# Optimization experiments

Measured on AMD Instinct MI355X. Metric: run time of the kernel, lower is better.

## Reference

```python
import jax, jax.numpy as jnp
import numpy as np

C_IN = 256
C_OUT = 256


def setup_inputs() -> dict:
    key = jax.random.key(0)
    k1, k2, k3, k4, k5 = jax.random.split(key, 5)
    B, C, H, W = 4, C_IN, 64, 64
    x = jax.random.normal(k1, (B, C, H, W), dtype=jnp.float32)
    y = jax.random.normal(k2, (B, C, H, W), dtype=jnp.float32)
    s = 1.0 / np.sqrt(C_IN)  # kaiming-ish init scale for 1x1 conv
    wq = jax.random.normal(k3, (C_OUT, C_IN), dtype=jnp.float32) * s
    wk = jax.random.normal(k4, (C_OUT, C_IN), dtype=jnp.float32) * s
    wv = jax.random.normal(k5, (C_OUT, C_IN), dtype=jnp.float32) * s
    gamma = jnp.ones((1,), dtype=jnp.float32) * 0.1
    return {"x": x, "y": y, "wq": wq, "wk": wk, "wv": wv, "gamma": gamma}


def reference(x, y, wq, wk, wv, gamma):
    B, C, H, W = x.shape
    N = H * W
    xf = x.reshape(B, C, N)  # [B, C, N]
    yf = y.reshape(B, C, N)
    q = jnp.einsum('oc,bcn->bno', wq, xf)   # [B, N, Co]
    k = jnp.einsum('oc,bcn->bon', wk, yf)   # [B, Co, N]
    v = jnp.einsum('oc,bcn->bon', wv, yf)   # [B, Co, N]
    energy = jnp.einsum('bio,boj->bij', q, k)          # [B, N, N]
    attention = jax.nn.softmax(energy, axis=-1)
    out = jnp.einsum('bcj,bij->bci', v, attention)     # [B, Co, N]
    out = out.reshape(B, -1, H, W)
    return gamma[0] * out + x
```

## Files before the change

kernel.cpp:

```cpp
#include <hip/hip_runtime.h>
#include <hip/hip_bf16.h>
#include <stdint.h>

#define C_DIM 256
#define N_DIM 4096
#define B_DIM 4

typedef __attribute__((ext_vector_type(8))) short s16x8;
typedef __attribute__((ext_vector_type(4))) short s16x4;
typedef __attribute__((ext_vector_type(4))) float f32x4;
typedef __attribute__((ext_vector_type(16))) float f32x16;
typedef __attribute__((ext_vector_type(4))) int i32x4;

static __device__ __forceinline__ short f2bs(float f) {
    __bf16 h = (__bf16)f;
    return __builtin_bit_cast(short, h);
}
static __device__ __forceinline__ float bs2f(short s) {
    unsigned int u = ((unsigned int)(unsigned short)s) << 16;
    return __builtin_bit_cast(float, u);
}
static __device__ __forceinline__ unsigned cvtpk(float lo, float hi) {
    unsigned r;
    asm("v_cvt_pk_bf16_f32 %0, %1, %2" : "=v"(r) : "v"(lo), "v"(hi));
    return r;
}
static __device__ __forceinline__ void plswap(unsigned &a, unsigned &b) {
    asm("v_permlane32_swap_b32 %0, %1" : "+v"(a), "+v"(b));
}

__global__ __launch_bounds__(256)
void prep_kernel(const float* __restrict__ x, const float* __restrict__ y,
                 const float* __restrict__ wq, const float* __restrict__ wk,
                 const float* __restrict__ wv,
                 short* __restrict__ xT, short* __restrict__ yT,
                 short* __restrict__ wb)
{
    int bid = blockIdx.x;
    int t = threadIdx.x;
    if (bid < 2048) {
        const float* src = (bid < 1024) ? x : y;
        short* dst = (bid < 1024) ? xT : yT;
        int id = bid & 1023;
        int ct = id & 3;
        int nt = (id >> 2) & 63;
        int b  = id >> 8;
        int n0 = nt * 64, c0 = ct * 64;
        __shared__ short T[64][66];
        int l = t & 63;
        int wv_ = t >> 6;
        #pragma unroll
        for (int p = 0; p < 16; ++p) {
            int c = wv_ + p * 4;
            float v = src[((size_t)(b * C_DIM + c0 + c)) * N_DIM + n0 + l];
            T[l][c] = f2bs(v);
        }
        __syncthreads();
        #pragma unroll
        for (int p = 0; p < 16; ++p) {
            int n = wv_ + p * 4;
            dst[((size_t)(b * N_DIM + n0 + n)) * C_DIM + c0 + l] = T[n][l];
        }
    } else {
        int id = bid - 2048;
        const float* w = (id < 32) ? wq : (id < 64) ? wk : wv;
        short* dst = wb + (size_t)(id / 32) * (C_DIM * C_DIM);
        int off = (id & 31) * 2048 + t * 8;
        f32x4 a  = *(const f32x4*)(w + off);
        f32x4 b4 = *(const f32x4*)(w + off + 4);
        s16x8 r;
        r[0]=f2bs(a[0]);  r[1]=f2bs(a[1]);  r[2]=f2bs(a[2]);  r[3]=f2bs(a[3]);
        r[4]=f2bs(b4[0]); r[5]=f2bs(b4[1]); r[6]=f2bs(b4[2]); r[7]=f2bs(b4[3]);
        *(s16x8*)(dst + off) = r;
    }
}

__global__ __launch_bounds__(256)
void proj_kernel(const short* __restrict__ xT, const short* __restrict__ yT,
                 const short* __restrict__ wb,
                 short* __restrict__ Qb, short* __restrict__ Kb,
                 short* __restrict__ Vb)
{
    int bid = blockIdx.x;
    int ot = bid & 3;
    int nt = (bid >> 2) & 63;
    int bp = bid >> 8;
    int b = bp / 3, p = bp % 3;
    int n0 = nt * 64, o0 = ot * 64;
    const short* src = (p == 0) ? xT : yT;
    const short* w = wb + (size_t)p * C_DIM * C_DIM;

    __shared__ __align__(16) short Xs[64][264];
    __shared__ __align__(16) short Ws[64][264];

    int t = threadIdx.x;
    const short* srcb = src + (size_t)(b * N_DIM + n0) * C_DIM;
    const short* wsrc = w + (size_t)o0 * C_DIM;
    #pragma unroll
    for (int pas = 0; pas < 8; ++pas) {
        int slot = pas * 256 + t;
        int row = slot >> 5, ck = slot & 31;
        *(s16x8*)&Xs[row][ck * 8] = *(const s16x8*)&srcb[(size_t)row * C_DIM + ck * 8];
        *(s16x8*)&Ws[row][ck * 8] = *(const s16x8*)&wsrc[(size_t)row * C_DIM + ck * 8];
    }
    __syncthreads();

    int lane = t & 63;
    int wid = t >> 6;
    int m = lane & 15, q = lane >> 4;
    f32x4 acc[4] = {};

    if (p < 2) {
        #pragma unroll
        for (int kk = 0; kk < 8; ++kk) {
            s16x8 af = *(const s16x8*)&Xs[wid * 16 + m][kk * 32 + q * 8];
            #pragma unroll
            for (int ob = 0; ob < 4; ++ob) {
                s16x8 bf = *(const s16x8*)&Ws[ob * 16 + m][kk * 32 + q * 8];
                acc[ob] = __builtin_amdgcn_mfma_f32_16x16x32_bf16(af, bf, acc[ob], 0, 0, 0);
            }
        }
        float sc = (p == 0) ? 1.4426950408889634f : 1.0f;
        short* dst = ((p == 0) ? Qb : Kb) + (size_t)b * N_DIM * C_DIM;
        #pragma unroll
        for (int ob = 0; ob < 4; ++ob)
            #pragma unroll
            for (int r = 0; r < 4; ++r) {
                int n = n0 + wid * 16 + q * 4 + r;
                int o = o0 + ob * 16 + m;
                dst[(size_t)n * C_DIM + o] = f2bs(acc[ob][r] * sc);
            }
    } else {
        #pragma unroll
        for (int kk = 0; kk < 8; ++kk) {
            s16x8 af = *(const s16x8*)&Ws[wid * 16 + m][kk * 32 + q * 8];
            #pragma unroll
            for (int nb = 0; nb < 4; ++nb) {
                s16x8 bf = *(const s16x8*)&Xs[nb * 16 + m][kk * 32 + q * 8];
                acc[nb] = __builtin_amdgcn_mfma_f32_16x16x32_bf16(af, bf, acc[nb], 0, 0, 0);
            }
        }
        short* dst = Vb + (size_t)b * C_DIM * N_DIM;
        #pragma unroll
        for (int nb = 0; nb < 4; ++nb)
            #pragma unroll
            for (int r = 0; r < 4; ++r) {
                int o = o0 + wid * 16 + q * 4 + r;
                int n = n0 + nb * 16 + m;
                dst[(size_t)o * N_DIM + n] = f2bs(acc[nb][r]);
            }
    }
}

__global__ __launch_bounds__(256, 2)
void attn_kernel(const short* __restrict__ Qb, const short* __restrict__ Kb,
                 const short* __restrict__ Vb,
                 short* __restrict__ Op01, short* __restrict__ Op23,
                 float* __restrict__ ms)
{
    int bid0 = blockIdx.x;
    int swz = (bid0 & 7) * 64 + (bid0 >> 3);
    int b  = swz >> 7;
    int ks = (swz >> 5) & 3;
    int qt = swz & 31;
    int i0 = qt * 128;

    int t = threadIdx.x;
    int wv = t >> 6;
    int lane = t & 63;
    int il = lane & 31, hi = lane >> 5;
    int q0 = i0 + wv * 32;

    __shared__ __align__(16) short Ksh[32][264];
    __shared__ __align__(16) short Vsh[256][40];

    const short* Qp = Qb + (size_t)b * N_DIM * C_DIM;
    const short* Kp = Kb + (size_t)b * N_DIM * C_DIM + (size_t)(ks * 1024) * C_DIM;
    const short* Vp = Vb + (size_t)b * C_DIM * N_DIM + ks * 1024;

    s16x8 qf[16];
    {
        const short* qrow = Qp + (size_t)(q0 + il) * C_DIM + hi * 8;
        #pragma unroll
        for (int kk = 0; kk < 16; ++kk)
            qf[kk] = *(const s16x8*)&qrow[kk * 16];
    }

    int krb = t >> 5, kck = t & 31;
    int vrb = t >> 2, vck = t & 3;

    {
        s16x8 kr[4], vr[4];
        #pragma unroll
        for (int p = 0; p < 4; ++p)
            kr[p] = *(const s16x8*)&Kp[(size_t)(p * 8 + krb) * C_DIM + kck * 8];
        #pragma unroll
        for (int p = 0; p < 4; ++p)
            vr[p] = *(const s16x8*)&Vp[(size_t)(p * 64 + vrb) * N_DIM + vck * 8];
        #pragma unroll
        for (int p = 0; p < 4; ++p) *(s16x8*)&Ksh[p * 8 + krb][kck * 8] = kr[p];
        #pragma unroll
        for (int p = 0; p < 4; ++p) *(s16x8*)&Vsh[p * 64 + vrb][vck * 8] = vr[p];
    }
    __syncthreads();

    f32x16 acc[8] = {};
    float srun = 0.f;

    for (int jt = 0; jt < 32; ++jt) {
        bool pfch = (jt < 31);

        f32x16 sv0 = {}, sv1 = {};
        __builtin_amdgcn_s_setprio(1);
        #pragma unroll
        for (int kk = 0; kk < 8; ++kk) {
            s16x8 a0 = *(const s16x8*)&Ksh[il][kk * 16 + hi * 8];
            sv0 = __builtin_amdgcn_mfma_f32_32x32x16_bf16(a0, qf[kk], sv0, 0, 0, 0);
            s16x8 a1 = *(const s16x8*)&Ksh[il][(kk + 8) * 16 + hi * 8];
            sv1 = __builtin_amdgcn_mfma_f32_32x32x16_bf16(a1, qf[kk + 8], sv1, 0, 0, 0);
        }
        __builtin_amdgcn_s_setprio(0);

        s16x8 kr[4];
        if (pfch) {
            const short* kg = Kp + (size_t)((jt + 1) * 32) * C_DIM;
            #pragma unroll
            for (int p = 0; p < 4; ++p)
                kr[p] = *(const s16x8*)&kg[(size_t)(p * 8 + krb) * C_DIM + kck * 8];
        }

        #pragma unroll
        for (int r = 0; r < 16; ++r) {
            float pe = exp2f((sv0[r] + sv1[r]) - 64.f);
            sv0[r] = pe;
            srun += pe;
        }

        unsigned d0[4], d1[4];
        #pragma unroll
        for (int rq = 0; rq < 4; ++rq) {
            d0[rq] = cvtpk(sv0[4 * rq + 0], sv0[4 * rq + 1]);
            d1[rq] = cvtpk(sv0[4 * rq + 2], sv0[4 * rq + 3]);
        }
        unsigned w0a = d0[0], w2a = d0[1]; plswap(w0a, w2a);
        unsigned w1a = d1[0], w3a = d1[1]; plswap(w1a, w3a);
        unsigned w0b = d0[2], w2b = d0[3]; plswap(w0b, w2b);
        unsigned w1b = d1[2], w3b = d1[3]; plswap(w1b, w3b);
        i32x4 pi0 = { (int)w0a, (int)w1a, (int)w2a, (int)w3a };
        i32x4 pi1 = { (int)w0b, (int)w1b, (int)w2b, (int)w3b };
        s16x8 pf0 = __builtin_bit_cast(s16x8, pi0);
        s16x8 pf1 = __builtin_bit_cast(s16x8, pi1);

        s16x8 vr[4];
        if (pfch) {
            const short* vg = Vp + (jt + 1) * 32;
            #pragma unroll
            for (int p = 0; p < 4; ++p)
                vr[p] = *(const s16x8*)&vg[(size_t)(p * 64 + vrb) * N_DIM + vck * 8];
        }

        __builtin_amdgcn_s_setprio(1);
        #pragma unroll
        for (int cs = 0; cs < 8; ++cs) {
            s16x8 va = *(const s16x8*)&Vsh[cs * 32 + il][hi * 8];
            acc[cs] = __builtin_amdgcn_mfma_f32_32x32x16_bf16(va, pf0, acc[cs], 0, 0, 0);
            s16x8 vb = *(const s16x8*)&Vsh[cs * 32 + il][16 + hi * 8];
            acc[cs] = __builtin_amdgcn_mfma_f32_32x32x16_bf16(vb, pf1, acc[cs], 0, 0, 0);
        }
        __builtin_amdgcn_s_setprio(0);

        __syncthreads();
        if (pfch) {
            #pragma unroll
            for (int p = 0; p < 4; ++p) *(s16x8*)&Ksh[p * 8 + krb][kck * 8] = kr[p];
            #pragma unroll
            for (int p = 0; p < 4; ++p) *(s16x8*)&Vsh[p * 64 + vrb][vck * 8] = vr[p];
        }
        __syncthreads();
    }

    srun += __shfl_xor(srun, 32, 64);
    int i = q0 + il;
    const size_t HSZ = (size_t)B_DIM * C_DIM * N_DIM;
    if (ks < 2) {
        short* o = Op01 + (size_t)ks * HSZ + (size_t)(b * C_DIM) * N_DIM + i;
        #pragma unroll
        for (int cs = 0; cs < 8; ++cs)
            #pragma unroll
            for (int r = 0; r < 16; ++r) {
                int c = cs * 32 + (r & 3) + 8 * (r >> 2) + 4 * hi;
                o[(size_t)c * N_DIM] = f2bs(acc[cs][r]);
            }
    } else {
        short* o = Op23 + ((size_t)(b * C_DIM) * N_DIM + i) * 2 + (ks - 2);
        #pragma unroll
        for (int cs = 0; cs < 8; ++cs)
            #pragma unroll
            for (int r = 0; r < 16; ++r) {
                int c = cs * 32 + (r & 3) + 8 * (r >> 2) + 4 * hi;
                o[(size_t)c * N_DIM * 2] = f2bs(acc[cs][r]);
            }
    }
    if (hi == 0) {
        float* msp = ms + (size_t)(ks * B_DIM + b) * N_DIM;
        msp[i] = srun;
    }
}

__global__ __launch_bounds__(256)
void merge_kernel(const short* __restrict__ Op01, const short* Op23,
                  const float* __restrict__ ms, const float* __restrict__ x,
                  const float* __restrict__ gamma, float* out)
{
    size_t base = ((size_t)blockIdx.x * 256 + threadIdx.x) * 8;
    int n = (int)(base & (N_DIM - 1));
    int b = (int)(base >> 20);
    const size_t HSZ = (size_t)B_DIM * C_DIM * N_DIM;

    s16x8 o0 = *(const s16x8*)&Op01[base];
    s16x8 o1 = *(const s16x8*)&Op01[HSZ + base];
    s16x8 pa = *(const s16x8*)&Op23[base * 2];
    s16x8 pb = *(const s16x8*)&Op23[base * 2 + 8];

    f32x4 den[2] = {};
    #pragma unroll
    for (int h = 0; h < 4; ++h) {
        const float* msp = ms + (size_t)(h * B_DIM + b) * N_DIM + n;
        f32x4 sa = *(const f32x4*)&msp[0];
        f32x4 sb = *(const f32x4*)&msp[4];
        #pragma unroll
        for (int e = 0; e < 4; ++e) { den[0][e] += sa[e]; den[1][e] += sb[e]; }
    }
    f32x4 xa = *(const f32x4*)&x[base];
    f32x4 xb = *(const f32x4*)&x[base + 4];
    float g = gamma[0];

    float res[8];
    #pragma unroll
    for (int e = 0; e < 8; ++e) {
        int half = e >> 2, e4 = e & 3;
        float o2 = bs2f(e < 4 ? pa[2 * e]     : pb[2 * (e - 4)]);
        float o3 = bs2f(e < 4 ? pa[2 * e + 1] : pb[2 * (e - 4) + 1]);
        float num = bs2f(o0[e]) + bs2f(o1[e]) + o2 + o3;
        float xv = (e < 4) ? xa[e4] : xb[e4];
        res[e] = g * (num / den[half][e4]) + xv;
    }
    f32x4 ra = { res[0], res[1], res[2], res[3] };
    f32x4 rb = { res[4], res[5], res[6], res[7] };
    *(f32x4*)&out[base] = ra;
    *(f32x4*)&out[base + 4] = rb;
}

extern "C" void kernel_launch(void* const* d_in, const int* in_sizes, int n_in,
                              void* d_out, int out_size, void* d_ws, size_t ws_size,
                              hipStream_t stream) {
    const float* x  = (const float*)d_in[0];
    const float* y  = (const float*)d_in[1];
    const float* wq = (const float*)d_in[2];
    const float* wk = (const float*)d_in[3];
    const float* wv = (const float*)d_in[4];
    const float* gm = (const float*)d_in[5];
    float* out = (float*)d_out;

    char* ws = (char*)d_ws;
    const size_t SZ = (size_t)B_DIM * N_DIM * C_DIM * sizeof(short);
    short* xT = (short*)(ws);
    short* yT = (short*)(ws + SZ);
    short* Qb = (short*)(ws + 2 * SZ);
    short* Kb = (short*)(ws + 3 * SZ);
    short* Vb = (short*)(ws + 4 * SZ);
    short* wb = (short*)(ws + 5 * SZ);
    float* ms = (float*)(ws + 5 * SZ);

    prep_kernel<<<dim3(2048 + 96), dim3(256), 0, stream>>>(x, y, wq, wk, wv, xT, yT, wb);
    proj_kernel<<<dim3(3072), dim3(256), 0, stream>>>(xT, yT, wb, Qb, Kb, Vb);
    attn_kernel<<<dim3(512), dim3(256), 0, stream>>>(Qb, Kb, Vb, xT, (short*)out, ms);
    merge_kernel<<<dim3(2048), dim3(256), 0, stream>>>(xT, (const short*)out, ms, x, gm, out);
}
```

Before: 128.2 us.

## Fuse fp32-to-bf16 transpose prep into projection kernel, loop over output tiles

```diff
diff --git a/kernel.cpp b/kernel.cpp
--- a/kernel.cpp
+++ b/kernel.cpp
@@ -30,125 +30,106 @@
 }
 
 __global__ __launch_bounds__(256)
-void prep_kernel(const float* __restrict__ x, const float* __restrict__ y,
+void proj_kernel(const float* __restrict__ x, const float* __restrict__ y,
                  const float* __restrict__ wq, const float* __restrict__ wk,
                  const float* __restrict__ wv,
-                 short* __restrict__ xT, short* __restrict__ yT,
-                 short* __restrict__ wb)
-{
-    int bid = blockIdx.x;
-    int t = threadIdx.x;
-    if (bid < 2048) {
-        const float* src = (bid < 1024) ? x : y;
-        short* dst = (bid < 1024) ? xT : yT;
-        int id = bid & 1023;
-        int ct = id & 3;
-        int nt = (id >> 2) & 63;
-        int b  = id >> 8;
-        int n0 = nt * 64, c0 = ct * 64;
-        __shared__ short T[64][66];
-        int l = t & 63;
-        int wv_ = t >> 6;
-        #pragma unroll
-        for (int p = 0; p < 16; ++p) {
-            int c = wv_ + p * 4;
-            float v = src[((size_t)(b * C_DIM + c0 + c)) * N_DIM + n0 + l];
-            T[l][c] = f2bs(v);
-        }
-        __syncthreads();
-        #pragma unroll
-        for (int p = 0; p < 16; ++p) {
-            int n = wv_ + p * 4;
-            dst[((size_t)(b * N_DIM + n0 + n)) * C_DIM + c0 + l] = T[n][l];
-        }
-    } else {
-        int id = bid - 2048;
-        const float* w = (id < 32) ? wq : (id < 64) ? wk : wv;
-        short* dst = wb + (size_t)(id / 32) * (C_DIM * C_DIM);
-        int off = (id & 31) * 2048 + t * 8;
-        f32x4 a  = *(const f32x4*)(w + off);
-        f32x4 b4 = *(const f32x4*)(w + off + 4);
-        s16x8 r;
-        r[0]=f2bs(a[0]);  r[1]=f2bs(a[1]);  r[2]=f2bs(a[2]);  r[3]=f2bs(a[3]);
-        r[4]=f2bs(b4[0]); r[5]=f2bs(b4[1]); r[6]=f2bs(b4[2]); r[7]=f2bs(b4[3]);
-        *(s16x8*)(dst + off) = r;
-    }
-}
-
-__global__ __launch_bounds__(256)
-void proj_kernel(const short* __restrict__ xT, const short* __restrict__ yT,
-                 const short* __restrict__ wb,
                  short* __restrict__ Qb, short* __restrict__ Kb,
                  short* __restrict__ Vb)
 {
     int bid = blockIdx.x;
-    int ot = bid & 3;
-    int nt = (bid >> 2) & 63;
-    int bp = bid >> 8;
-    int b = bp / 3, p = bp % 3;
-    int n0 = nt * 64, o0 = ot * 64;
-    const short* src = (p == 0) ? xT : yT;
-    const short* w = wb + (size_t)p * C_DIM * C_DIM;
+    int nt = bid & 63;
+    int b  = (bid >> 6) & 3;
+    int p  = bid >> 8;
+    int n0 = nt * 64;
+    const float* src = (p == 0) ? x : y;
+    const float* w   = (p == 0) ? wq : (p == 1) ? wk : wv;
 
     __shared__ __align__(16) short Xs[64][264];
     __shared__ __align__(16) short Ws[64][264];
+    __shared__ short T[64][66];
 
     int t = threadIdx.x;
-    const short* srcb = src + (size_t)(b * N_DIM + n0) * C_DIM;
-    const short* wsrc = w + (size_t)o0 * C_DIM;
-    #pragma unroll
-    for (int pas = 0; pas < 8; ++pas) {
-        int slot = pas * 256 + t;
-        int row = slot >> 5, ck = slot & 31;
-        *(s16x8*)&Xs[row][ck * 8] = *(const s16x8*)&srcb[(size_t)row * C_DIM + ck * 8];
-        *(s16x8*)&Ws[row][ck * 8] = *(const s16x8*)&wsrc[(size_t)row * C_DIM + ck * 8];
-    }
-    __syncthreads();
+    int l = t & 63;
+    int wv_ = t >> 6;
+
+    for (int ct = 0; ct < 4; ++ct) {
+        #pragma unroll
+        for (int pp = 0; pp < 16; ++pp) {
+            int c = wv_ + pp * 4;
+            float v = src[((size_t)(b * C_DIM + ct * 64 + c)) * N_DIM + n0 + l];
+            T[l][c] = f2bs(v);
+        }
+        __syncthreads();
+        #pragma unroll
+        for (int pp = 0; pp < 16; ++pp) {
+            int n = wv_ + pp * 4;
+            Xs[n][ct * 64 + l] = T[n][l];
+        }
+        __syncthreads();
+    }
 
     int lane = t & 63;
     int wid = t >> 6;
     int m = lane & 15, q = lane >> 4;
-    f32x4 acc[4] = {};
-
-    if (p < 2) {
-        #pragma unroll
-        for (int kk = 0; kk < 8; ++kk) {
-            s16x8 af = *(const s16x8*)&Xs[wid * 16 + m][kk * 32 + q * 8];
-            #pragma unroll
-            for (int ob = 0; ob < 4; ++ob) {
-                s16x8 bf = *(const s16x8*)&Ws[ob * 16 + m][kk * 32 + q * 8];
-                acc[ob] = __builtin_amdgcn_mfma_f32_16x16x32_bf16(af, bf, acc[ob], 0, 0, 0);
+
+    for (int ot = 0; ot < 4; ++ot) {
+        int o0 = ot * 64;
+        #pragma unroll
+        for (int pas = 0; pas < 8; ++pas) {
+            int slot = pas * 256 + t;
+            int row = slot >> 5, ck = slot & 31;
+            const float* wr = &w[(size_t)(o0 + row) * C_DIM + ck * 8];
+            f32x4 a  = *(const f32x4*)wr;
+            f32x4 b4 = *(const f32x4*)(wr + 4);
+            s16x8 r;
+            r[0]=f2bs(a[0]);  r[1]=f2bs(a[1]);  r[2]=f2bs(a[2]);  r[3]=f2bs(a[3]);
+            r[4]=f2bs(b4[0]); r[5]=f2bs(b4[1]); r[6]=f2bs(b4[2]); r[7]=f2bs(b4[3]);
+            *(s16x8*)&Ws[row][ck * 8] = r;
+        }
+        __syncthreads();
+
+        f32x4 acc[4] = {};
+        if (p < 2) {
+            #pragma unroll
+            for (int kk = 0; kk < 8; ++kk) {
+                s16x8 af = *(const s16x8*)&Xs[wid * 16 + m][kk * 32 + q * 8];
+                #pragma unroll
+                for (int ob = 0; ob < 4; ++ob) {
+                    s16x8 bf = *(const s16x8*)&Ws[ob * 16 + m][kk * 32 + q * 8];
+                    acc[ob] = __builtin_amdgcn_mfma_f32_16x16x32_bf16(af, bf, acc[ob], 0, 0, 0);
+                }
             }
-        }
-        float sc = (p == 0) ? 1.4426950408889634f : 1.0f;
-        short* dst = ((p == 0) ? Qb : Kb) + (size_t)b * N_DIM * C_DIM;
-        #pragma unroll
-        for (int ob = 0; ob < 4; ++ob)
-            #pragma unroll
-            for (int r = 0; r < 4; ++r) {
-                int n = n0 + wid * 16 + q * 4 + r;
-                int o = o0 + ob * 16 + m;
-                dst[(size_t)n * C_DIM + o] = f2bs(acc[ob][r] * sc);
+            float sc = (p == 0) ? 1.4426950408889634f : 1.0f;
+            short* dst = ((p == 0) ? Qb : Kb) + (size_t)b * N_DIM * C_DIM;
+            #pragma unroll
+            for (int ob = 0; ob < 4; ++ob)
+                #pragma unroll
+                for (int r = 0; r < 4; ++r) {
+                    int n = n0 + wid * 16 + q * 4 + r;
+                    int o = o0 + ob * 16 + m;
+                    dst[(size_t)n * C_DIM + o] = f2bs(acc[ob][r] * sc);
+                }
+        } else {
+            #pragma unroll
+            for (int kk = 0; kk < 8; ++kk) {
+                s16x8 af = *(const s16x8*)&Ws[wid * 16 + m][kk * 32 + q * 8];
+                #pragma unroll
+                for (int nb = 0; nb < 4; ++nb) {
+                    s16x8 bf = *(const s16x8*)&Xs[nb * 16 + m][kk * 32 + q * 8];
+                    acc[nb] = __builtin_amdgcn_mfma_f32_16x16x32_bf16(af, bf, acc[nb], 0, 0, 0);
+                }
             }
-    } else {
-        #pragma unroll
-        for (int kk = 0; kk < 8; ++kk) {
-            s16x8 af = *(const s16x8*)&Ws[wid * 16 + m][kk * 32 + q * 8];
-            #pragma unroll
-            for (int nb = 0; nb < 4; ++nb) {
-                s16x8 bf = *(const s16x8*)&Xs[nb * 16 + m][kk * 32 + q * 8];
-                acc[nb] = __builtin_amdgcn_mfma_f32_16x16x32_bf16(af, bf, acc[nb], 0, 0, 0);
-            }
-        }
-        short* dst = Vb + (size_t)b * C_DIM * N_DIM;
-        #pragma unroll
-        for (int nb = 0; nb < 4; ++nb)
-            #pragma unroll
-            for (int r = 0; r < 4; ++r) {
-                int o = o0 + wid * 16 + q * 4 + r;
-                int n = n0 + nb * 16 + m;
-                dst[(size_t)o * N_DIM + n] = f2bs(acc[nb][r]);
-            }
+            short* dst = Vb + (size_t)b * C_DIM * N_DIM;
+            #pragma unroll
+            for (int nb = 0; nb < 4; ++nb)
+                #pragma unroll
+                for (int r = 0; r < 4; ++r) {
+                    int o = o0 + wid * 16 + q * 4 + r;
+                    int n = n0 + nb * 16 + m;
+                    dst[(size_t)o * N_DIM + n] = f2bs(acc[nb][r]);
+                }
+        }
+        __syncthreads();
     }
 }
 
@@ -364,16 +345,13 @@
 
     char* ws = (char*)d_ws;
     const size_t SZ = (size_t)B_DIM * N_DIM * C_DIM * sizeof(short);
-    short* xT = (short*)(ws);
-    short* yT = (short*)(ws + SZ);
     short* Qb = (short*)(ws + 2 * SZ);
     short* Kb = (short*)(ws + 3 * SZ);
     short* Vb = (short*)(ws + 4 * SZ);
-    short* wb = (short*)(ws + 5 * SZ);
+    short* Op01 = (short*)ws;
     float* ms = (float*)(ws + 5 * SZ);
 
-    prep_kernel<<<dim3(2048 + 96), dim3(256), 0, stream>>>(x, y, wq, wk, wv, xT, yT, wb);
-    proj_kernel<<<dim3(3072), dim3(256), 0, stream>>>(xT, yT, wb, Qb, Kb, Vb);
-    attn_kernel<<<dim3(512), dim3(256), 0, stream>>>(Qb, Kb, Vb, xT, (short*)out, ms);
-    merge_kernel<<<dim3(2048), dim3(256), 0, stream>>>(xT, (const short*)out, ms, x, gm, out);
-}
+    proj_kernel<<<dim3(768), dim3(256), 0, stream>>>(x, y, wq, wk, wv, Qb, Kb, Vb);
+    attn_kernel<<<dim3(512), dim3(256), 0, stream>>>(Qb, Kb, Vb, Op01, (short*)out, ms);
+    merge_kernel<<<dim3(2048), dim3(256), 0, stream>>>(Op01, (const short*)out, ms, x, gm, out);
+}
```

Measured after the change: 125.4 us. -2.2%, faster.
